# Optimization experiments

Hardware: AMD Instinct MI355X
Metric: run time of the kernel (lower is better)

## Reference

```python
import jax, jax.numpy as jnp
import numpy as np

def setup_inputs() -> dict:
    key = jax.random.key(0)
    QKV = jax.random.normal(key, (3, 2, 8, 4096, 64), dtype=jnp.float32)
    return {"QKV": QKV}

def reference(QKV):
    Q, K, V = QKV[0], QKV[1], QKV[2]            # each [B, H, N, d]
    scores = jnp.einsum('bhnd,bhmd->bhnm', Q, K)  # full N x N score matrix (no scaling, matching source)
    attn = jax.nn.softmax(scores, axis=-1)
    return jnp.einsum('bhnm,bhmd->bhnd', attn, V)
```

## Files before the change

### kernel.cpp

```cpp
#include <hip/hip_runtime.h>


typedef _Float16 f16x8 __attribute__((ext_vector_type(8)));
typedef _Float16 f16x2 __attribute__((ext_vector_type(2)));
typedef short s16x8 __attribute__((ext_vector_type(8)));
typedef short s16x4 __attribute__((ext_vector_type(4)));
typedef float f32x4 __attribute__((ext_vector_type(4)));

#define NHEADS 16
#define SEQ 4096
#define HDIM 64
#define BR 256
#define NH 4
#define BC 64
#define KP 72
#define PP 72
#define NSPLIT 2
#define MPAD 4.0f

__device__ __forceinline__ float fast_exp2(float x) {
#if __has_builtin(__builtin_amdgcn_exp2f)
  return __builtin_amdgcn_exp2f(x);
#else
  return exp2f(x);
#endif
}

__device__ __forceinline__ f16x2 pkrtz(float a, float b) {
  return __builtin_bit_cast(f16x2, __builtin_amdgcn_cvt_pkrtz(a, b));
}

__device__ __forceinline__ unsigned short f2bf(float f) {
  unsigned u = __builtin_bit_cast(unsigned, f);
  u += 0x7fffu + ((u >> 16) & 1u);
  return (unsigned short)(u >> 16);
}

__device__ __forceinline__ unsigned bfpack2(float a, float b) {
  return (__builtin_bit_cast(unsigned, b) & 0xffff0000u) |
         (__builtin_bit_cast(unsigned, a) >> 16);
}

__global__ __launch_bounds__(256) void prep(const float* __restrict__ QKV,
                                            _Float16* __restrict__ K16,
                                            short* __restrict__ Vt) {
  const size_t tensElems = (size_t)NHEADS * SEQ * HDIM;
  __shared__ __align__(16) short T[64 * KP];
  if (blockIdx.x < 2048) {
    const float* Kf = QKV + tensElems;
    size_t i = ((size_t)blockIdx.x * 256 + threadIdx.x) * 8;
    float4 a = *(const float4*)(Kf + i);
    float4 b = *(const float4*)(Kf + i + 4);
    union { f16x8 v; f16x2 h2[4]; } u;
    u.h2[0] = pkrtz(a.x, a.y);
    u.h2[1] = pkrtz(a.z, a.w);
    u.h2[2] = pkrtz(b.x, b.y);
    u.h2[3] = pkrtz(b.z, b.w);
    *(f16x8*)(K16 + i) = u.v;
  } else {
    const int vb = blockIdx.x - 2048;
    const int bh = vb >> 6;
    const int nt = vb & 63;
    const float* Vh = QKV + 2 * tensElems + (size_t)bh * SEQ * HDIM +
                      (size_t)nt * 64 * HDIM;
    const int t = threadIdx.x;
    #pragma unroll
    for (int p = 0; p < 4; ++p) {
      int idx = t + p * 256;
      int row = idx >> 4, c4 = (idx & 15) << 2;
      float4 v = *(const float4*)(Vh + row * HDIM + c4);
      s16x4 h;
      h[0] = (short)f2bf(v.x); h[1] = (short)f2bf(v.y);
      h[2] = (short)f2bf(v.z); h[3] = (short)f2bf(v.w);
      *(s16x4*)&T[row * KP + c4] = h;
    }
    __syncthreads();
    const int d = t & 63, w = t >> 6;
    s16x8 o0, o1;
    #pragma unroll
    for (int j = 0; j < 8; ++j) o0[j] = T[(w * 16 + j) * KP + d];
    #pragma unroll
    for (int j = 0; j < 8; ++j) o1[j] = T[(w * 16 + 8 + j) * KP + d];
    short* out = Vt + (size_t)bh * HDIM * SEQ + (size_t)d * SEQ + nt * 64 + w * 16;
    *(s16x8*)out = o0;
    *(s16x8*)(out + 8) = o1;
  }
}

__global__ __launch_bounds__(256) void combine2(const _Float16* __restrict__ Op,
                                                const float2* __restrict__ Ml,
                                                float* __restrict__ O) {
  const size_t tensElems = (size_t)NHEADS * SEQ * HDIM;
  size_t t = (size_t)blockIdx.x * 256 + threadIdx.x;
  size_t row = t >> 3;
  int seg = (int)(t & 7) << 3;
  float2 s0 = Ml[row];
  float2 s1 = Ml[(size_t)NHEADS * SEQ + row];
  float Ms = fmaxf(s0.x, s1.x);
  float a0 = fast_exp2(s0.x - Ms) * s0.y;
  float a1 = fast_exp2(s1.x - Ms) * s1.y;
  float inv = 1.0f / (a0 + a1);
  a0 *= inv;
  a1 *= inv;
  f16x8 o0 = *(const f16x8*)(Op + row * HDIM + seg);
  f16x8 o1 = *(const f16x8*)(Op + tensElems + row * HDIM + seg);
  float4 r0, r1;
  r0.x = (float)o0[0] * a0 + (float)o1[0] * a1;
  r0.y = (float)o0[1] * a0 + (float)o1[1] * a1;
  r0.z = (float)o0[2] * a0 + (float)o1[2] * a1;
  r0.w = (float)o0[3] * a0 + (float)o1[3] * a1;
  r1.x = (float)o0[4] * a0 + (float)o1[4] * a1;
  r1.y = (float)o0[5] * a0 + (float)o1[5] * a1;
  r1.z = (float)o0[6] * a0 + (float)o1[6] * a1;
  r1.w = (float)o0[7] * a0 + (float)o1[7] * a1;
  *(float4*)(O + row * HDIM + seg) = r0;
  *(float4*)(O + row * HDIM + seg + 4) = r1;
}

template <bool PRE, bool SPLIT>
__global__ __launch_bounds__(256, 2) void flash_attn(const float* __restrict__ QKV,
                                                     const _Float16* __restrict__ K16g,
                                                     const short* __restrict__ Vt16,
                                                     float* __restrict__ Out,
                                                     _Float16* __restrict__ Opart,
                                                     float2* __restrict__ Ml) {
  const size_t headElems = (size_t)SEQ * HDIM;
  const size_t tensElems = (size_t)NHEADS * headElems;
  const int bh = blockIdx.x & 15;
  const int qt = blockIdx.x >> 4;
  const int split = SPLIT ? blockIdx.y : 0;
  const int ktBeg = SPLIT ? split * (SEQ / BC / NSPLIT) : 0;
  const int ktN = SPLIT ? (SEQ / BC / NSPLIT) : (SEQ / BC);

  const float* Q = QKV + (size_t)bh * headElems;
  const float* Kf = QKV + tensElems + (size_t)bh * headElems;
  const float* Vf = QKV + 2 * tensElems + (size_t)bh * headElems;
  const _Float16* Kg16 = K16g + (size_t)bh * headElems;
  const short* Vg16 = Vt16 + (size_t)bh * headElems;
  float* O = Out + (size_t)bh * headElems;

  const int tid = threadIdx.x;
  const int wave = tid >> 6;
  const int lane = tid & 63;
  const int g = lane >> 4;
  const int l16 = lane & 15;

  __shared__ __align__(16) _Float16 Ks[BC * KP];
  __shared__ __align__(16) short Vs[HDIM * KP];
  __shared__ __align__(16) short Ps[4][NH][16 * PP];

  const float LOG2E = 1.4426950408889634f;
  const int qbase = qt * BR + wave * (16 * NH);
  f16x8 qf[NH][2];
  #pragma unroll
  for (int h = 0; h < NH; ++h) {
    const float* qp = Q + (size_t)(qbase + h * 16 + l16) * HDIM + g * 8;
    #pragma unroll
    for (int c = 0; c < 2; ++c) {
      float4 a = *(const float4*)(qp + c * 32);
      float4 b = *(const float4*)(qp + c * 32 + 4);
      union { f16x8 v; f16x2 h2[4]; } u;
      u.h2[0] = pkrtz(a.x * LOG2E, a.y * LOG2E);
      u.h2[1] = pkrtz(a.z * LOG2E, a.w * LOG2E);
      u.h2[2] = pkrtz(b.x * LOG2E, b.y * LOG2E);
      u.h2[3] = pkrtz(b.z * LOG2E, b.w * LOG2E);
      qf[h][c] = u.v;
    }
  }

  const int sr = tid >> 2;
  const int sc = (tid & 3) << 4;

  s16x8 kpre[2];
  s16x8 vpre[2];

  auto prefetch = [&](int kt) {
    if constexpr (PRE) {
      const _Float16* kg = Kg16 + (size_t)(kt * BC + sr) * HDIM + sc;
      kpre[0] = *(const s16x8*)(kg);
      kpre[1] = *(const s16x8*)(kg + 8);
      const short* vg = Vg16 + (size_t)sr * SEQ + kt * BC + sc;
      vpre[0] = *(const s16x8*)(vg);
      vpre[1] = *(const s16x8*)(vg + 8);
    }
  };
  auto commit = [&](int kt) {
    if constexpr (PRE) {
      *(s16x8*)&Ks[sr * KP + sc] = kpre[0];
      *(s16x8*)&Ks[sr * KP + sc + 8] = kpre[1];
      *(s16x8*)&Vs[sr * KP + sc] = vpre[0];
      *(s16x8*)&Vs[sr * KP + sc + 8] = vpre[1];
    } else {
      const float* kg = Kf + (size_t)(kt * BC + sr) * HDIM + sc;
      float4 a = *(const float4*)(kg), b = *(const float4*)(kg + 4);
      float4 c = *(const float4*)(kg + 8), d = *(const float4*)(kg + 12);
      union { f16x8 v; f16x2 h2[4]; } ka, kb;
      ka.h2[0] = pkrtz(a.x, a.y);
      ka.h2[1] = pkrtz(a.z, a.w);
      ka.h2[2] = pkrtz(b.x, b.y);
      ka.h2[3] = pkrtz(b.z, b.w);
      kb.h2[0] = pkrtz(c.x, c.y);
      kb.h2[1] = pkrtz(c.z, c.w);
      kb.h2[2] = pkrtz(d.x, d.y);
      kb.h2[3] = pkrtz(d.z, d.w);
      *(f16x8*)&Ks[sr * KP + sc] = ka.v;
      *(f16x8*)&Ks[sr * KP + sc + 8] = kb.v;
      const float* vg = Vf + (size_t)(kt * BC + sr) * HDIM + sc;
      float4 va = *(const float4*)(vg), vb = *(const float4*)(vg + 4);
      float4 vc = *(const float4*)(vg + 8), vd = *(const float4*)(vg + 12);
      float vv[16] = {va.x, va.y, va.z, va.w, vb.x, vb.y, vb.z, vb.w,
                      vc.x, vc.y, vc.z, vc.w, vd.x, vd.y, vd.z, vd.w};
      #pragma unroll
      for (int j = 0; j < 16; ++j) Vs[(sc + j) * KP + sr] = (short)f2bf(vv[j]);
    }
  };

  f32x4 acc[NH][4];
  #pragma unroll
  for (int h = 0; h < NH; ++h)
    #pragma unroll
    for (int nt = 0; nt < 4; ++nt)
      #pragma unroll
      for (int i = 0; i < 4; ++i) acc[h][nt][i] = 0.f;
  float l_[NH] = {0.f, 0.f, 0.f, 0.f};
  float negM[NH] = {0.f, 0.f, 0.f, 0.f};

  prefetch(ktBeg);
  commit(ktBeg);

  for (int it = 0; it < ktN; ++it) {
    const int kt = ktBeg + it;
    __syncthreads();
    if (it < ktN - 1) prefetch(kt + 1);

    f32x4 s[NH][4];
    #pragma unroll
    for (int jt = 0; jt < 4; ++jt) {
      const int ka = (jt * 16 + l16) * KP + g * 8;
      f16x8 k0 = *(const f16x8*)&Ks[ka];
      f16x8 k1 = *(const f16x8*)&Ks[ka + 32];
      #pragma unroll
      for (int h = 0; h < NH; ++h) {
        f32x4 z;
        z[0] = z[1] = z[2] = z[3] = negM[h];
        z = __builtin_amdgcn_mfma_f32_16x16x32_f16(k0, qf[h][0], z, 0, 0, 0);
        z = __builtin_amdgcn_mfma_f32_16x16x32_f16(k1, qf[h][1], z, 0, 0, 0);
        s[h][jt] = z;
      }
    }

    if (it == 0) {
      #pragma unroll
      for (int h = 0; h < NH; ++h) {
        float mx = s[h][0][0];
        #pragma unroll
        for (int jt = 0; jt < 4; ++jt)
          #pragma unroll
          for (int ri = 0; ri < 4; ++ri) mx = fmaxf(mx, s[h][jt][ri]);
        mx = fmaxf(mx, __shfl_xor(mx, 16));
        mx = fmaxf(mx, __shfl_xor(mx, 32));
        negM[h] = -(mx + MPAD);
        #pragma unroll
        for (int jt = 0; jt < 4; ++jt)
          #pragma unroll
          for (int ri = 0; ri < 4; ++ri) s[h][jt][ri] += negM[h];
      }
    }

    #pragma unroll
    for (int h = 0; h < NH; ++h) {
      float psum = l_[h];
      const int e0 = l16 * PP + 4 * g;
      #pragma unroll
      for (int jt = 0; jt < 4; ++jt) {
        float p0 = fast_exp2(s[h][jt][0]);
        float p1 = fast_exp2(s[h][jt][1]);
        float p2 = fast_exp2(s[h][jt][2]);
        float p3 = fast_exp2(s[h][jt][3]);
        psum += (p0 + p1) + (p2 + p3);
        uint2 w;
        w.x = bfpack2(p0, p1);
        w.y = bfpack2(p2, p3);
        *(uint2*)&Ps[wave][h][e0 + jt * 16] = w;
      }
      l_[h] = psum;
    }

    s16x8 pa[NH][2];
    #pragma unroll
    for (int h = 0; h < NH; ++h) {
      pa[h][0] = *(const s16x8*)&Ps[wave][h][l16 * PP + g * 8];
      pa[h][1] = *(const s16x8*)&Ps[wave][h][l16 * PP + g * 8 + 32];
    }
    #pragma unroll
    for (int nt = 0; nt < 4; ++nt) {
      const int va = (nt * 16 + l16) * KP + g * 8;
      s16x8 v0 = *(const s16x8*)&Vs[va];
      s16x8 v1 = *(const s16x8*)&Vs[va + 32];
      #pragma unroll
      for (int h = 0; h < NH; ++h) {
        acc[h][nt] = __builtin_amdgcn_mfma_f32_16x16x32_bf16(pa[h][0], v0, acc[h][nt], 0, 0, 0);
        acc[h][nt] = __builtin_amdgcn_mfma_f32_16x16x32_bf16(pa[h][1], v1, acc[h][nt], 0, 0, 0);
      }
    }

    __syncthreads();
    if (it < ktN - 1) commit(kt + 1);
  }

  #pragma unroll
  for (int h = 0; h < NH; ++h) {
    float lf = l_[h];
    lf += __shfl_xor(lf, 16);
    lf += __shfl_xor(lf, 32);
    float linv = 1.0f / lf;
    if constexpr (SPLIT) {
      if (g == 0) {
        Ml[(size_t)split * NHEADS * SEQ + (size_t)bh * SEQ + qbase + h * 16 + l16] =
            float2{-negM[h], lf};
      }
      _Float16* op = Opart + (size_t)split * tensElems + (size_t)bh * headElems;
      #pragma unroll
      for (int ri = 0; ri < 4; ++ri) {
        float lB = __shfl(linv, 4 * g + ri);
        const int row = qbase + h * 16 + 4 * g + ri;
        #pragma unroll
        for (int nt = 0; nt < 4; ++nt)
          op[(size_t)row * HDIM + nt * 16 + l16] = (_Float16)(acc[h][nt][ri] * lB);
      }
    } else {
      #pragma unroll
      for (int ri = 0; ri < 4; ++ri) {
        float lB = __shfl(linv, 4 * g + ri);
        const int row = qbase + h * 16 + 4 * g + ri;
        #pragma unroll
        for (int nt = 0; nt < 4; ++nt)
          O[(size_t)row * HDIM + nt * 16 + l16] = acc[h][nt][ri] * lB;
      }
    }
  }
}

extern "C" void kernel_launch(void* const* d_in, const int* in_sizes, int n_in,
                              void* d_out, int out_size, void* d_ws, size_t ws_size,
                              hipStream_t stream) {
  const float* QKV = (const float*)d_in[0];
  float* Out = (float*)d_out;
  const size_t tensElems = (size_t)NHEADS * SEQ * HDIM;
  const size_t k16Bytes = tensElems * sizeof(_Float16);
  const size_t vtBytes = tensElems * sizeof(short);
  const size_t opBytes = (size_t)NSPLIT * tensElems * sizeof(_Float16);
  const size_t mlBytes = (size_t)NSPLIT * NHEADS * SEQ * 8;

  dim3 block(256);

  if (ws_size >= k16Bytes + vtBytes + opBytes + mlBytes) {
    _Float16* K16 = (_Float16*)d_ws;
    short* Vt16 = (short*)((char*)d_ws + k16Bytes);
    _Float16* Opart = (_Float16*)((char*)d_ws + k16Bytes + vtBytes);
    float2* Ml = (float2*)((char*)d_ws + k16Bytes + vtBytes + opBytes);
    hipLaunchKernelGGL(prep, dim3(3072), block, 0, stream, QKV, K16, Vt16);
    hipLaunchKernelGGL((flash_attn<true, true>), dim3(NHEADS * (SEQ / BR), NSPLIT),
                       block, 0, stream, QKV, K16, Vt16, Out, Opart, Ml);
    hipLaunchKernelGGL(combine2, dim3((NHEADS * SEQ * HDIM / 8) / 256), block, 0,
                       stream, Opart, Ml, Out);
  } else {
    hipLaunchKernelGGL((flash_attn<false, false>), dim3(NHEADS * (SEQ / BR)), block,
                       0, stream, QKV, (const _Float16*)nullptr,
                       (const short*)nullptr, Out, (_Float16*)nullptr,
                       (float2*)nullptr);
  }
}
```

Baseline: 169.6 us.

## Keep P in registers, double-buffer K/V LDS, swizzle K, and split KV four ways

The P matrix now goes straight from the QK MFMA output registers into the PV MFMA operand layout. This removes the per-wave LDS round trip for P and the old Ps buffer, and relies on a permuted K row order (rbase) plus an XOR swizzle to match the layouts. K/V shared tiles are double-buffered, which drops the second __syncthreads per iteration, and occupancy hints rise to 3 blocks per CU. The KV split goes from 2 to 4 with a generic combine kernel, giving more parallelism at the cost of more partial-output traffic. The first tile's max is now computed in a separate extra QK pass.

```diff
diff --git a/kernel.cpp b/kernel.cpp
--- a/kernel.cpp
+++ b/kernel.cpp
@@ -6,6 +6,7 @@
 typedef short s16x8 __attribute__((ext_vector_type(8)));
 typedef short s16x4 __attribute__((ext_vector_type(4)));
 typedef float f32x4 __attribute__((ext_vector_type(4)));
+typedef unsigned u32x4 __attribute__((ext_vector_type(4)));
 
 #define NHEADS 16
 #define SEQ 4096
@@ -14,8 +15,6 @@
 #define NH 4
 #define BC 64
 #define KP 72
-#define PP 72
-#define NSPLIT 2
 #define MPAD 4.0f
 
 __device__ __forceinline__ float fast_exp2(float x) {
@@ -87,38 +86,42 @@
   }
 }
 
-__global__ __launch_bounds__(256) void combine2(const _Float16* __restrict__ Op,
+template <int NS>
+__global__ __launch_bounds__(256) void combineN(const _Float16* __restrict__ Op,
                                                 const float2* __restrict__ Ml,
                                                 float* __restrict__ O) {
   const size_t tensElems = (size_t)NHEADS * SEQ * HDIM;
   size_t t = (size_t)blockIdx.x * 256 + threadIdx.x;
   size_t row = t >> 3;
   int seg = (int)(t & 7) << 3;
-  float2 s0 = Ml[row];
-  float2 s1 = Ml[(size_t)NHEADS * SEQ + row];
-  float Ms = fmaxf(s0.x, s1.x);
-  float a0 = fast_exp2(s0.x - Ms) * s0.y;
-  float a1 = fast_exp2(s1.x - Ms) * s1.y;
-  float inv = 1.0f / (a0 + a1);
-  a0 *= inv;
-  a1 *= inv;
-  f16x8 o0 = *(const f16x8*)(Op + row * HDIM + seg);
-  f16x8 o1 = *(const f16x8*)(Op + tensElems + row * HDIM + seg);
-  float4 r0, r1;
-  r0.x = (float)o0[0] * a0 + (float)o1[0] * a1;
-  r0.y = (float)o0[1] * a0 + (float)o1[1] * a1;
-  r0.z = (float)o0[2] * a0 + (float)o1[2] * a1;
-  r0.w = (float)o0[3] * a0 + (float)o1[3] * a1;
-  r1.x = (float)o0[4] * a0 + (float)o1[4] * a1;
-  r1.y = (float)o0[5] * a0 + (float)o1[5] * a1;
-  r1.z = (float)o0[6] * a0 + (float)o1[6] * a1;
-  r1.w = (float)o0[7] * a0 + (float)o1[7] * a1;
+  float2 s[NS];
+  #pragma unroll
+  for (int i = 0; i < NS; ++i) s[i] = Ml[(size_t)i * NHEADS * SEQ + row];
+  float Ms = s[0].x;
+  #pragma unroll
+  for (int i = 1; i < NS; ++i) Ms = fmaxf(Ms, s[i].x);
+  float a[NS], tot = 0.f;
+  #pragma unroll
+  for (int i = 0; i < NS; ++i) {
+    a[i] = fast_exp2(s[i].x - Ms) * s[i].y;
+    tot += a[i];
+  }
+  float inv = 1.0f / tot;
+  float r[8] = {0.f, 0.f, 0.f, 0.f, 0.f, 0.f, 0.f, 0.f};
+  #pragma unroll
+  for (int i = 0; i < NS; ++i) {
+    f16x8 o = *(const f16x8*)(Op + (size_t)i * tensElems + row * HDIM + seg);
+    float w = a[i] * inv;
+    #pragma unroll
+    for (int j = 0; j < 8; ++j) r[j] += (float)o[j] * w;
+  }
+  float4 r0{r[0], r[1], r[2], r[3]}, r1{r[4], r[5], r[6], r[7]};
   *(float4*)(O + row * HDIM + seg) = r0;
   *(float4*)(O + row * HDIM + seg + 4) = r1;
 }
 
 template <bool PRE, bool SPLIT>
-__global__ __launch_bounds__(256, 2) void flash_attn(const float* __restrict__ QKV,
+__global__ __launch_bounds__(256, 3) void flash_attn(const float* __restrict__ QKV,
                                                      const _Float16* __restrict__ K16g,
                                                      const short* __restrict__ Vt16,
                                                      float* __restrict__ Out,
@@ -129,8 +132,9 @@
   const int bh = blockIdx.x & 15;
   const int qt = blockIdx.x >> 4;
   const int split = SPLIT ? blockIdx.y : 0;
-  const int ktBeg = SPLIT ? split * (SEQ / BC / NSPLIT) : 0;
-  const int ktN = SPLIT ? (SEQ / BC / NSPLIT) : (SEQ / BC);
+  const int nsp = SPLIT ? (int)gridDim.y : 1;
+  const int ktN = (SEQ / BC) / nsp;
+  const int ktBeg = split * ktN;
 
   const float* Q = QKV + (size_t)bh * headElems;
   const float* Kf = QKV + tensElems + (size_t)bh * headElems;
@@ -145,9 +149,8 @@
   const int g = lane >> 4;
   const int l16 = lane & 15;
 
-  __shared__ __align__(16) _Float16 Ks[BC * KP];
-  __shared__ __align__(16) short Vs[HDIM * KP];
-  __shared__ __align__(16) short Ps[4][NH][16 * PP];
+  __shared__ __align__(16) _Float16 KsB[2][BC * KP];
+  __shared__ __align__(16) short VsB[2][HDIM * KP];
 
   const float LOG2E = 1.4426950408889634f;
   const int qbase = qt * BR + wave * (16 * NH);
@@ -168,8 +171,14 @@
     }
   }
 
+  const int rbase = 8 * (l16 >> 2) + 4 * (l16 & 1) + ((l16 >> 1) & 1);
+  const int swz = ((g ^ (l16 >> 2)) << 3);
+
   const int sr = tid >> 2;
   const int sc = (tid & 3) << 4;
+  const int qw = (sr >> 3) & 3;
+  const int kc0 = ((((tid & 3) << 1) + 0) ^ qw) << 3;
+  const int kc1 = ((((tid & 3) << 1) + 1) ^ qw) << 3;
 
   s16x8 kpre[2];
   s16x8 vpre[2];
@@ -184,12 +193,14 @@
       vpre[1] = *(const s16x8*)(vg + 8);
     }
   };
-  auto commit = [&](int kt) {
+  auto commit = [&](int buf, int kt) {
+    _Float16* Kd = KsB[buf];
+    short* Vd = VsB[buf];
     if constexpr (PRE) {
-      *(s16x8*)&Ks[sr * KP + sc] = kpre[0];
-      *(s16x8*)&Ks[sr * KP + sc + 8] = kpre[1];
-      *(s16x8*)&Vs[sr * KP + sc] = vpre[0];
-      *(s16x8*)&Vs[sr * KP + sc + 8] = vpre[1];
+      *(s16x8*)&Kd[sr * KP + kc0] = kpre[0];
+      *(s16x8*)&Kd[sr * KP + kc1] = kpre[1];
+      *(s16x8*)&Vd[sr * KP + sc] = vpre[0];
+      *(s16x8*)&Vd[sr * KP + sc + 8] = vpre[1];
     } else {
       const float* kg = Kf + (size_t)(kt * BC + sr) * HDIM + sc;
       float4 a = *(const float4*)(kg), b = *(const float4*)(kg + 4);
@@ -203,15 +214,15 @@
       kb.h2[1] = pkrtz(c.z, c.w);
       kb.h2[2] = pkrtz(d.x, d.y);
       kb.h2[3] = pkrtz(d.z, d.w);
-      *(f16x8*)&Ks[sr * KP + sc] = ka.v;
-      *(f16x8*)&Ks[sr * KP + sc + 8] = kb.v;
+      *(f16x8*)&Kd[sr * KP + kc0] = ka.v;
+      *(f16x8*)&Kd[sr * KP + kc1] = kb.v;
       const float* vg = Vf + (size_t)(kt * BC + sr) * HDIM + sc;
       float4 va = *(const float4*)(vg), vb = *(const float4*)(vg + 4);
       float4 vc = *(const float4*)(vg + 8), vd = *(const float4*)(vg + 12);
       float vv[16] = {va.x, va.y, va.z, va.w, vb.x, vb.y, vb.z, vb.w,
                       vc.x, vc.y, vc.z, vc.w, vd.x, vd.y, vd.z, vd.w};
       #pragma unroll
-      for (int j = 0; j < 16; ++j) Vs[(sc + j) * KP + sr] = (short)f2bf(vv[j]);
+      for (int j = 0; j < 16; ++j) Vd[(sc + j) * KP + sr] = (short)f2bf(vv[j]);
     }
   };
 
@@ -226,86 +237,79 @@
   float negM[NH] = {0.f, 0.f, 0.f, 0.f};
 
   prefetch(ktBeg);
-  commit(ktBeg);
+  commit(0, ktBeg);
+  int cur = 0;
 
   for (int it = 0; it < ktN; ++it) {
-    const int kt = ktBeg + it;
     __syncthreads();
-    if (it < ktN - 1) prefetch(kt + 1);
-
-    f32x4 s[NH][4];
+    if (it + 1 < ktN) prefetch(ktBeg + it + 1);
+    const _Float16* Kb = KsB[cur];
+    const short* Vb = VsB[cur];
+
+    if (it == 0) {
+      float mx[NH];
+      #pragma unroll
+      for (int h = 0; h < NH; ++h) mx[h] = -3.0e38f;
+      #pragma unroll
+      for (int jt = 0; jt < 4; ++jt) {
+        const int ka = (rbase + ((jt >> 1) << 5) + ((jt & 1) << 1)) * KP + swz;
+        f16x8 k0 = *(const f16x8*)&Kb[ka];
+        f16x8 k1 = *(const f16x8*)&Kb[ka + 32];
+        #pragma unroll
+        for (int h = 0; h < NH; ++h) {
+          f32x4 z;
+          z[0] = z[1] = z[2] = z[3] = 0.f;
+          z = __builtin_amdgcn_mfma_f32_16x16x32_f16(k0, qf[h][0], z, 0, 0, 0);
+          z = __builtin_amdgcn_mfma_f32_16x16x32_f16(k1, qf[h][1], z, 0, 0, 0);
+          mx[h] = fmaxf(mx[h], fmaxf(fmaxf(z[0], z[1]), fmaxf(z[2], z[3])));
+        }
+      }
+      #pragma unroll
+      for (int h = 0; h < NH; ++h) {
+        float m2 = fmaxf(mx[h], __shfl_xor(mx[h], 16));
+        m2 = fmaxf(m2, __shfl_xor(m2, 32));
+        negM[h] = -(m2 + MPAD);
+      }
+    }
+
+    u32x4 Wp[NH][2];
     #pragma unroll
     for (int jt = 0; jt < 4; ++jt) {
-      const int ka = (jt * 16 + l16) * KP + g * 8;
-      f16x8 k0 = *(const f16x8*)&Ks[ka];
-      f16x8 k1 = *(const f16x8*)&Ks[ka + 32];
+      const int ka = (rbase + ((jt >> 1) << 5) + ((jt & 1) << 1)) * KP + swz;
+      f16x8 k0 = *(const f16x8*)&Kb[ka];
+      f16x8 k1 = *(const f16x8*)&Kb[ka + 32];
       #pragma unroll
       for (int h = 0; h < NH; ++h) {
         f32x4 z;
         z[0] = z[1] = z[2] = z[3] = negM[h];
         z = __builtin_amdgcn_mfma_f32_16x16x32_f16(k0, qf[h][0], z, 0, 0, 0);
         z = __builtin_amdgcn_mfma_f32_16x16x32_f16(k1, qf[h][1], z, 0, 0, 0);
-        s[h][jt] = z;
-      }
-    }
-
-    if (it == 0) {
-      #pragma unroll
-      for (int h = 0; h < NH; ++h) {
-        float mx = s[h][0][0];
-        #pragma unroll
-        for (int jt = 0; jt < 4; ++jt)
-          #pragma unroll
-          for (int ri = 0; ri < 4; ++ri) mx = fmaxf(mx, s[h][jt][ri]);
-        mx = fmaxf(mx, __shfl_xor(mx, 16));
-        mx = fmaxf(mx, __shfl_xor(mx, 32));
-        negM[h] = -(mx + MPAD);
-        #pragma unroll
-        for (int jt = 0; jt < 4; ++jt)
-          #pragma unroll
-          for (int ri = 0; ri < 4; ++ri) s[h][jt][ri] += negM[h];
-      }
-    }
-
-    #pragma unroll
-    for (int h = 0; h < NH; ++h) {
-      float psum = l_[h];
-      const int e0 = l16 * PP + 4 * g;
-      #pragma unroll
-      for (int jt = 0; jt < 4; ++jt) {
-        float p0 = fast_exp2(s[h][jt][0]);
-        float p1 = fast_exp2(s[h][jt][1]);
-        float p2 = fast_exp2(s[h][jt][2]);
-        float p3 = fast_exp2(s[h][jt][3]);
-        psum += (p0 + p1) + (p2 + p3);
-        uint2 w;
-        w.x = bfpack2(p0, p1);
-        w.y = bfpack2(p2, p3);
-        *(uint2*)&Ps[wave][h][e0 + jt * 16] = w;
-      }
-      l_[h] = psum;
-    }
-
-    s16x8 pa[NH][2];
-    #pragma unroll
-    for (int h = 0; h < NH; ++h) {
-      pa[h][0] = *(const s16x8*)&Ps[wave][h][l16 * PP + g * 8];
-      pa[h][1] = *(const s16x8*)&Ps[wave][h][l16 * PP + g * 8 + 32];
-    }
+        float p0 = fast_exp2(z[0]);
+        float p1 = fast_exp2(z[1]);
+        float p2 = fast_exp2(z[2]);
+        float p3 = fast_exp2(z[3]);
+        l_[h] += (p0 + p1) + (p2 + p3);
+        Wp[h][jt >> 1][(jt & 1)] = bfpack2(p0, p2);
+        Wp[h][jt >> 1][(jt & 1) + 2] = bfpack2(p1, p3);
+      }
+    }
+
     #pragma unroll
     for (int nt = 0; nt < 4; ++nt) {
       const int va = (nt * 16 + l16) * KP + g * 8;
-      s16x8 v0 = *(const s16x8*)&Vs[va];
-      s16x8 v1 = *(const s16x8*)&Vs[va + 32];
+      s16x8 v0 = *(const s16x8*)&Vb[va];
+      s16x8 v1 = *(const s16x8*)&Vb[va + 32];
       #pragma unroll
       for (int h = 0; h < NH; ++h) {
-        acc[h][nt] = __builtin_amdgcn_mfma_f32_16x16x32_bf16(pa[h][0], v0, acc[h][nt], 0, 0, 0);
-        acc[h][nt] = __builtin_amdgcn_mfma_f32_16x16x32_bf16(pa[h][1], v1, acc[h][nt], 0, 0, 0);
-      }
-    }
-
-    __syncthreads();
-    if (it < ktN - 1) commit(kt + 1);
+        s16x8 pa0 = __builtin_bit_cast(s16x8, Wp[h][0]);
+        s16x8 pa1 = __builtin_bit_cast(s16x8, Wp[h][1]);
+        acc[h][nt] = __builtin_amdgcn_mfma_f32_16x16x32_bf16(pa0, v0, acc[h][nt], 0, 0, 0);
+        acc[h][nt] = __builtin_amdgcn_mfma_f32_16x16x32_bf16(pa1, v1, acc[h][nt], 0, 0, 0);
+      }
+    }
+
+    if (it + 1 < ktN) commit(cur ^ 1, ktBeg + it + 1);
+    cur ^= 1;
   }
 
   #pragma unroll
@@ -349,21 +353,31 @@
   const size_t tensElems = (size_t)NHEADS * SEQ * HDIM;
   const size_t k16Bytes = tensElems * sizeof(_Float16);
   const size_t vtBytes = tensElems * sizeof(short);
-  const size_t opBytes = (size_t)NSPLIT * tensElems * sizeof(_Float16);
-  const size_t mlBytes = (size_t)NSPLIT * NHEADS * SEQ * 8;
+  const size_t mlUnit = (size_t)NHEADS * SEQ * sizeof(float2);
+  const size_t need4 = k16Bytes + vtBytes + 4 * tensElems * 2 + 4 * mlUnit;
+  const size_t need2 = k16Bytes + vtBytes + 2 * tensElems * 2 + 2 * mlUnit;
 
   dim3 block(256);
-
-  if (ws_size >= k16Bytes + vtBytes + opBytes + mlBytes) {
-    _Float16* K16 = (_Float16*)d_ws;
-    short* Vt16 = (short*)((char*)d_ws + k16Bytes);
-    _Float16* Opart = (_Float16*)((char*)d_ws + k16Bytes + vtBytes);
-    float2* Ml = (float2*)((char*)d_ws + k16Bytes + vtBytes + opBytes);
+  _Float16* K16 = (_Float16*)d_ws;
+  short* Vt16 = (short*)((char*)d_ws + k16Bytes);
+  char* rest = (char*)d_ws + k16Bytes + vtBytes;
+
+  if (ws_size >= need4) {
+    _Float16* Opart = (_Float16*)rest;
+    float2* Ml = (float2*)(rest + 4 * tensElems * 2);
     hipLaunchKernelGGL(prep, dim3(3072), block, 0, stream, QKV, K16, Vt16);
-    hipLaunchKernelGGL((flash_attn<true, true>), dim3(NHEADS * (SEQ / BR), NSPLIT),
+    hipLaunchKernelGGL((flash_attn<true, true>), dim3(NHEADS * (SEQ / BR), 4),
                        block, 0, stream, QKV, K16, Vt16, Out, Opart, Ml);
-    hipLaunchKernelGGL(combine2, dim3((NHEADS * SEQ * HDIM / 8) / 256), block, 0,
-                       stream, Opart, Ml, Out);
+    hipLaunchKernelGGL((combineN<4>), dim3((NHEADS * SEQ * HDIM / 8) / 256), block,
+                       0, stream, Opart, Ml, Out);
+  } else if (ws_size >= need2) {
+    _Float16* Opart = (_Float16*)rest;
+    float2* Ml = (float2*)(rest + 2 * tensElems * 2);
+    hipLaunchKernelGGL(prep, dim3(3072), block, 0, stream, QKV, K16, Vt16);
+    hipLaunchKernelGGL((flash_attn<true, true>), dim3(NHEADS * (SEQ / BR), 2),
+                       block, 0, stream, QKV, K16, Vt16, Out, Opart, Ml);
+    hipLaunchKernelGGL((combineN<2>), dim3((NHEADS * SEQ * HDIM / 8) / 256), block,
+                       0, stream, Opart, Ml, Out);
   } else {
     hipLaunchKernelGGL((flash_attn<false, false>), dim3(NHEADS * (SEQ / BR)), block,
                        0, stream, QKV, (const _Float16*)nullptr,
```

Result: slower. 466.4 us (+175.0%).
